# Kernel optimization log

Measured on AMD Instinct MI355X. Metric: run time of the kernel, lower is better.

The kernel has to match this reference:

```python
import jax, jax.numpy as jnp
import numpy as np

N_ATOMS = 50000
DEG = 16                 # uniform neighbor count per atom
N_EDGES = N_ATOMS * DEG
NUM_ELEMENTS = 3
NUM_PAIRS = 6
EPS = 1e-12


def setup_inputs() -> dict:
    key = jax.random.key(0)
    k0, k1, k2, k3, k4 = jax.random.split(key, 5)
    positions = jax.random.normal(k0, (N_ATOMS, 3), jnp.float32) * 10.0
    # Uniform-degree edge list: every atom i is the source of exactly DEG edges.
    source = jnp.repeat(jnp.arange(N_ATOMS, dtype=jnp.int32), DEG)
    target = jax.random.randint(k1, (N_EDGES,), 0, N_ATOMS, jnp.int32)
    edge_index = jnp.stack([source, target])          # (2, E)
    element_indices = jax.random.randint(k2, (N_ATOMS,), 0, NUM_ELEMENTS, jnp.int32)
    # symmetric element-pair -> pair-index table
    plt = np.zeros((NUM_ELEMENTS, NUM_ELEMENTS), dtype=np.int32)
    p = 0
    for a in range(NUM_ELEMENTS):
        for b in range(a, NUM_ELEMENTS):
            plt[a, b] = plt[b, a] = p
            p += 1
    pair_lookup_table = jnp.asarray(plt)
    k_angle = jax.random.uniform(k3, (NUM_PAIRS,), jnp.float32) + 0.5
    cos0 = jax.random.uniform(k4, (NUM_PAIRS,), jnp.float32) * 2.0 - 1.0
    return {
        "positions": positions,
        "edge_index": edge_index,
        "element_indices": element_indices,
        "pair_lookup_table": pair_lookup_table,
        "k_angle": k_angle,
        "cos0": cos0,
        "num_atoms": N_ATOMS,
    }


def build_triplets(edge_index, num_atoms, max_deg):
    """Vectorized, jit-compatible version of ManyBodyPotential.build_triplets.

    Returns padded triplet arrays of shape (num_atoms*max_deg*max_deg,) plus a
    validity mask; valid entries match the torch per-atom-loop output exactly.
    """
    source, target = edge_index[0], edge_index[1]
    n_edges = source.shape[0]
    sort_idx = jnp.argsort(source, stable=True)       # CSR grouping by source
    sorted_target = target[sort_idx]
    counts = jax.ops.segment_sum(jnp.ones_like(source), source,
                                 num_segments=num_atoms)          # (N,)
    row_ptr = jnp.concatenate([jnp.zeros((1,), counts.dtype),
                               jnp.cumsum(counts)])               # (N+1,)
    slot = jnp.arange(max_deg, dtype=jnp.int32)
    gidx = row_ptr[:-1, None] + slot[None, :]          # (N, MAX_DEG)
    valid = slot[None, :] < counts[:, None]            # (N, MAX_DEG)
    safe = jnp.clip(gidx, 0, n_edges - 1)
    neigh_t = sorted_target[safe]                      # (N, MAX_DEG) neighbor atom ids
    neigh_e = sort_idx[safe].astype(jnp.int32)         # (N, MAX_DEG) original edge ids
    gj, gk = jnp.meshgrid(slot, slot, indexing='ij')   # (MAX_DEG, MAX_DEG)
    pair_ok = gj != gk
    mask = valid[:, gj] & valid[:, gk] & pair_ok[None]  # (N, MD, MD)
    tj = neigh_t[:, gj]
    tk = neigh_t[:, gk]
    eij = neigh_e[:, gj]
    eik = neigh_e[:, gk]
    ti = jnp.broadcast_to(jnp.arange(num_atoms, dtype=jnp.int32)[:, None, None],
                          mask.shape)
    flat = lambda a: a.reshape(-1)
    return flat(ti), flat(tj), flat(tk), flat(eij), flat(eik), flat(mask)


def reference(positions, edge_index, element_indices, pair_lookup_table,
              k_angle, cos0, num_atoms):
    ti, tj, tk, eij, eik, mask = build_triplets(edge_index, num_atoms, DEG)
    # Angular three-body energy: sum_t k_p * (cos(theta_jik) - cos0_p)^2
    r_ij = positions[tj] - positions[ti]               # (T, 3)
    r_ik = positions[tk] - positions[ti]               # (T, 3)
    dot = jnp.sum(r_ij * r_ik, axis=-1)
    n_ij = jnp.sqrt(jnp.sum(r_ij * r_ij, axis=-1))
    n_ik = jnp.sqrt(jnp.sum(r_ik * r_ik, axis=-1))
    cos_t = dot / (n_ij * n_ik + EPS)
    p = pair_lookup_table[element_indices[tj], element_indices[tk]]
    e_t = k_angle[p] * (cos_t - cos0[p]) ** 2
    energy = jnp.sum(jnp.where(mask, e_t, 0.0))
    return energy
```

## Files before the change

### kernel.cpp

```cpp
#include <hip/hip_runtime.h>

#define DEG 16
#define ATOMS_PER_BLOCK 16
#define NBLOCKS 2048
#define EPS_F 1e-12f

__global__ __launch_bounds__(256) void ManyBodyPotential_85143431675992_kernel(
    const float* __restrict__ pos,
    const int*   __restrict__ target,
    const int*   __restrict__ elem,
    const int*   __restrict__ plt,
    const float* __restrict__ k_angle,
    const float* __restrict__ cos0,
    float*       __restrict__ partials,
    float*       __restrict__ out,
    int n_atoms)
{
    __shared__ float  ka_tab[9];
    __shared__ float  c0_tab[9];
    __shared__ float4 s4[ATOMS_PER_BLOCK][DEG + 1];
    __shared__ int    se[ATOMS_PER_BLOCK][DEG + 1];
    __shared__ float  wsum[4];

    const int t = threadIdx.x;
    if (t < 9) {
        const int p = plt[t];
        ka_tab[t] = k_angle[p];
        c0_tab[t] = cos0[p];
    }

    const int a = t >> 4;
    const int j = t & 15;
    const int n_groups = (n_atoms + ATOMS_PER_BLOCK - 1) / ATOMS_PER_BLOCK;

    float acc = 0.0f;

    for (int g = blockIdx.x; g < n_groups; g += gridDim.x) {
        const int atom = g * ATOMS_PER_BLOCK + a;
        const bool active = (atom < n_atoms);

        float rx = 0.f, ry = 0.f, rz = 0.f, rn = 0.f;
        int   ej = 0;
        if (active) {
            const float pix = pos[atom * 3 + 0];
            const float piy = pos[atom * 3 + 1];
            const float piz = pos[atom * 3 + 2];
            const int   tj  = target[atom * DEG + j];
            rx = pos[tj * 3 + 0] - pix;
            ry = pos[tj * 3 + 1] - piy;
            rz = pos[tj * 3 + 2] - piz;
            rn = sqrtf(rx * rx + ry * ry + rz * rz);
            ej = elem[tj];
            s4[a][j] = make_float4(rx, ry, rz, rn);
            se[a][j] = ej;
        }
        __syncthreads();

        if (active) {
            const int ej3 = ej * 3;
            #pragma unroll
            for (int k = 0; k < DEG; ++k) {
                const float4 o  = s4[a][k];
                const int    ek = se[a][k];
                const float  dt = rx * o.x + ry * o.y + rz * o.z;
                const float  ct = dt / (rn * o.w + EPS_F);
                const int    idx = ej3 + ek;
                const float  d  = ct - c0_tab[idx];
                const float  e  = ka_tab[idx] * d * d;
                if (k != j) acc += e;
            }
        }
        __syncthreads();
    }

    #pragma unroll
    for (int off = 32; off > 0; off >>= 1)
        acc += __shfl_down(acc, off, 64);
    const int wave = t >> 6;
    if ((t & 63) == 0) wsum[wave] = acc;
    __syncthreads();
    if (t == 0) {
        const float s = wsum[0] + wsum[1] + wsum[2] + wsum[3];
        if (partials) partials[blockIdx.x] = s;
        else          atomicAdd(out, s);
    }
}

__global__ __launch_bounds__(512) void mbp_reduce_kernel(
    const float* __restrict__ partials, float* __restrict__ out, int n)
{
    __shared__ float wsum[8];
    const int t = threadIdx.x;
    float acc = 0.0f;
    for (int i = t; i < n; i += 512) acc += partials[i];
    #pragma unroll
    for (int off = 32; off > 0; off >>= 1)
        acc += __shfl_down(acc, off, 64);
    if ((t & 63) == 0) wsum[t >> 6] = acc;
    __syncthreads();
    if (t == 0) {
        float s = 0.0f;
        #pragma unroll
        for (int i = 0; i < 8; ++i) s += wsum[i];
        out[0] = s;
    }
}

__global__ void mbp_zero_kernel(float* out) {
    if (threadIdx.x == 0) out[0] = 0.0f;
}

extern "C" void kernel_launch(void* const* d_in, const int* in_sizes, int n_in,
                              void* d_out, int out_size, void* d_ws, size_t ws_size,
                              hipStream_t stream) {
    const float* pos     = (const float*)d_in[0];
    const int*   edge    = (const int*)d_in[1];
    const int*   elem    = (const int*)d_in[2];
    const int*   plt     = (const int*)d_in[3];
    const float* k_angle = (const float*)d_in[4];
    const float* cos0    = (const float*)d_in[5];
    float*       out     = (float*)d_out;

    const int n_atoms = in_sizes[0] / 3;
    const int n_edges = in_sizes[1] / 2;
    const int* target = edge + n_edges;

    const bool ws_ok = (d_ws != nullptr) && (ws_size >= NBLOCKS * sizeof(float));
    float* partials = ws_ok ? (float*)d_ws : nullptr;

    if (!ws_ok) mbp_zero_kernel<<<1, 64, 0, stream>>>(out);

    ManyBodyPotential_85143431675992_kernel<<<NBLOCKS, 256, 0, stream>>>(
        pos, target, elem, plt, k_angle, cos0, partials, out, n_atoms);

    if (ws_ok)
        mbp_reduce_kernel<<<1, 512, 0, stream>>>(partials, out, NBLOCKS);
}
```

Baseline: 81.16 us.

## Exploit pair symmetry with unit vectors and one block per atom group

Each edge vector is normalized once with rsqrt, so the inner loop needs only a dot product instead of a per-pair divide. Since the pair table is symmetric, each thread visits only the 8 following neighbors and doubles the first 7 terms, which halves the inner-loop work. The grid-stride loop is replaced by one block per 16-atom group, and the per-element k/cos0 row is held in registers and selected by compares instead of read from a shared-memory table. Dropping the EPS term and folding the element index into the float4 w slot can change results slightly for degenerate zero-length edges.

```diff
diff --git a/kernel.cpp b/kernel.cpp
--- a/kernel.cpp
+++ b/kernel.cpp
@@ -2,8 +2,6 @@
 
 #define DEG 16
 #define ATOMS_PER_BLOCK 16
-#define NBLOCKS 2048
-#define EPS_F 1e-12f
 
 __global__ __launch_bounds__(256) void ManyBodyPotential_85143431675992_kernel(
     const float* __restrict__ pos,
@@ -19,7 +17,6 @@
     __shared__ float  ka_tab[9];
     __shared__ float  c0_tab[9];
     __shared__ float4 s4[ATOMS_PER_BLOCK][DEG + 1];
-    __shared__ int    se[ATOMS_PER_BLOCK][DEG + 1];
     __shared__ float  wsum[4];
 
     const int t = threadIdx.x;
@@ -29,55 +26,54 @@
         c0_tab[t] = cos0[p];
     }
 
-    const int a = t >> 4;
-    const int j = t & 15;
-    const int n_groups = (n_atoms + ATOMS_PER_BLOCK - 1) / ATOMS_PER_BLOCK;
+    const int a    = t >> 4;
+    const int j    = t & 15;
+    const int atom = blockIdx.x * ATOMS_PER_BLOCK + a;
+    const bool active = (atom < n_atoms);
+
+    float ux = 0.f, uy = 0.f, uz = 0.f;
+    int   ej = 0;
+    if (active) {
+        const float pix = pos[atom * 3 + 0];
+        const float piy = pos[atom * 3 + 1];
+        const float piz = pos[atom * 3 + 2];
+        const int   tj  = target[atom * DEG + j];
+        const float dx  = pos[tj * 3 + 0] - pix;
+        const float dy  = pos[tj * 3 + 1] - piy;
+        const float dz  = pos[tj * 3 + 2] - piz;
+        const float r2  = dx * dx + dy * dy + dz * dz;
+        const float rinv = (r2 > 0.f) ? rsqrtf(r2) : 0.f;
+        ux = dx * rinv; uy = dy * rinv; uz = dz * rinv;
+        ej = elem[tj];
+        s4[a][j] = make_float4(ux, uy, uz, (float)ej);
+    }
+    __syncthreads();
 
     float acc = 0.0f;
+    if (active) {
+        const int   r   = ej * 3;
+        const float ka0 = ka_tab[r + 0], ka1 = ka_tab[r + 1], ka2 = ka_tab[r + 2];
+        const float c00 = c0_tab[r + 0], c01 = c0_tab[r + 1], c02 = c0_tab[r + 2];
 
-    for (int g = blockIdx.x; g < n_groups; g += gridDim.x) {
-        const int atom = g * ATOMS_PER_BLOCK + a;
-        const bool active = (atom < n_atoms);
-
-        float rx = 0.f, ry = 0.f, rz = 0.f, rn = 0.f;
-        int   ej = 0;
-        if (active) {
-            const float pix = pos[atom * 3 + 0];
-            const float piy = pos[atom * 3 + 1];
-            const float piz = pos[atom * 3 + 2];
-            const int   tj  = target[atom * DEG + j];
-            rx = pos[tj * 3 + 0] - pix;
-            ry = pos[tj * 3 + 1] - piy;
-            rz = pos[tj * 3 + 2] - piz;
-            rn = sqrtf(rx * rx + ry * ry + rz * rz);
-            ej = elem[tj];
-            s4[a][j] = make_float4(rx, ry, rz, rn);
-            se[a][j] = ej;
+        float acc2 = 0.0f, acc8 = 0.0f;
+        #pragma unroll
+        for (int d = 1; d <= 8; ++d) {
+            const int    k  = (j + d) & 15;
+            const float4 o  = s4[a][k];
+            const float  ka = (o.w == 1.0f) ? ka1 : ((o.w == 2.0f) ? ka2 : ka0);
+            const float  c0 = (o.w == 1.0f) ? c01 : ((o.w == 2.0f) ? c02 : c00);
+            const float  ct = ux * o.x + uy * o.y + uz * o.z;
+            const float  dd = ct - c0;
+            const float  e  = ka * dd * dd;
+            if (d < 8) acc2 += e; else acc8 = e;
         }
-        __syncthreads();
-
-        if (active) {
-            const int ej3 = ej * 3;
-            #pragma unroll
-            for (int k = 0; k < DEG; ++k) {
-                const float4 o  = s4[a][k];
-                const int    ek = se[a][k];
-                const float  dt = rx * o.x + ry * o.y + rz * o.z;
-                const float  ct = dt / (rn * o.w + EPS_F);
-                const int    idx = ej3 + ek;
-                const float  d  = ct - c0_tab[idx];
-                const float  e  = ka_tab[idx] * d * d;
-                if (k != j) acc += e;
-            }
-        }
-        __syncthreads();
+        acc = 2.0f * acc2 + acc8;
     }
 
     #pragma unroll
     for (int off = 32; off > 0; off >>= 1)
         acc += __shfl_down(acc, off, 64);
-    const int wave = t >> 6;
-    if ((t & 63) == 0) wsum[wave] = acc;
+    if ((t & 63) == 0) wsum[t >> 6] = acc;
     __syncthreads();
     if (t == 0) {
         const float s = wsum[0] + wsum[1] + wsum[2] + wsum[3];
@@ -86,13 +82,13 @@
     }
 }
 
-__global__ __launch_bounds__(512) void mbp_reduce_kernel(
+__global__ __launch_bounds__(1024) void mbp_reduce_kernel(
     const float* __restrict__ partials, float* __restrict__ out, int n)
 {
-    __shared__ float wsum[8];
+    __shared__ float wsum[16];
     const int t = threadIdx.x;
     float acc = 0.0f;
-    for (int i = t; i < n; i += 512) acc += partials[i];
+    for (int i = t; i < n; i += 1024) acc += partials[i];
     #pragma unroll
     for (int off = 32; off > 0; off >>= 1)
         acc += __shfl_down(acc, off, 64);
@@ -101,7 +97,7 @@
     if (t == 0) {
         float s = 0.0f;
         #pragma unroll
-        for (int i = 0; i < 8; ++i) s += wsum[i];
+        for (int i = 0; i < 16; ++i) s += wsum[i];
         out[0] = s;
     }
 }
@@ -125,14 +121,16 @@
     const int n_edges = in_sizes[1] / 2;
     const int* target = edge + n_edges;
 
-    const bool ws_ok = (d_ws != nullptr) && (ws_size >= NBLOCKS * sizeof(float));
+    const int n_blocks = (n_atoms + ATOMS_PER_BLOCK - 1) / ATOMS_PER_BLOCK;
+
+    const bool ws_ok = (d_ws != nullptr) && (ws_size >= (size_t)n_blocks * sizeof(float));
     float* partials = ws_ok ? (float*)d_ws : nullptr;
 
     if (!ws_ok) mbp_zero_kernel<<<1, 64, 0, stream>>>(out);
 
-    ManyBodyPotential_85143431675992_kernel<<<NBLOCKS, 256, 0, stream>>>(
+    ManyBodyPotential_85143431675992_kernel<<<n_blocks, 256, 0, stream>>>(
         pos, target, elem, plt, k_angle, cos0, partials, out, n_atoms);
 
     if (ws_ok)
-        mbp_reduce_kernel<<<1, 512, 0, stream>>>(partials, out, NBLOCKS);
+        mbp_reduce_kernel<<<1, 1024, 0, stream>>>(partials, out, n_blocks);
 }
```

After: 79.64 us. No clear change (-1.9%).
